# Kernel tuning notes

Measured on AMD Instinct MI355X. Metric: run time of the kernel, lower is better.

## Reference

```python
import jax, jax.numpy as jnp
import numpy as np

B, N, D = 4, 2048, 1024
H = 16
DH = D // H


def setup_inputs() -> dict:
    key = jax.random.key(0)
    ks = jax.random.split(key, 9)
    s_in = 1.0 / np.sqrt(D)
    x = jax.random.normal(ks[0], (B, N, D), dtype=jnp.float32)
    Wq = jax.random.uniform(ks[1], (D, D), jnp.float32, -s_in, s_in)
    bq = jax.random.uniform(ks[2], (D,), jnp.float32, -s_in, s_in)
    Wk = jax.random.uniform(ks[3], (D, D), jnp.float32, -s_in, s_in)
    bk = jax.random.uniform(ks[4], (D,), jnp.float32, -s_in, s_in)
    Wv = jax.random.uniform(ks[5], (D, D), jnp.float32, -s_in, s_in)
    bv = jax.random.uniform(ks[6], (D,), jnp.float32, -s_in, s_in)
    Wo = jax.random.uniform(ks[7], (D, D), jnp.float32, -s_in, s_in)
    bo = jax.random.uniform(ks[8], (D,), jnp.float32, -s_in, s_in)
    return {"x": x, "Wq": Wq, "bq": bq, "Wk": Wk, "bk": bk,
            "Wv": Wv, "bv": bv, "Wo": Wo, "bo": bo}


def reference(x, Wq, bq, Wk, bk, Wv, bv, Wo, bo):
    b, n, d = x.shape
    q = (x @ Wq + bq).reshape(b, n, H, DH)  # (b, n, h, dh)
    k = (x @ Wk + bk).reshape(b, n, H, DH)
    v = (x @ Wv + bv).reshape(b, n, H, DH)
    scale = 1.0 / jnp.sqrt(jnp.asarray(DH, x.dtype))
    scores = jnp.einsum("bqhd,bkhd->bhqk", q, k) * scale  # (b, h, n, n)
    # valid = arange(1..n) per query => causal mask: key index < valid[q] = q+1
    causal = jnp.arange(n)[None, :] <= jnp.arange(n)[:, None]  # (n_q, n_k)
    scores = jnp.where(causal[None, None, :, :], scores, -jnp.inf)
    weights = jax.nn.softmax(scores, axis=-1)
    out = jnp.einsum("bhqk,bkhd->bqhd", weights, v).reshape(b, n, d)
    return out @ Wo + bo
```

## Files before the change

### kernel.cpp

```cpp
#include <hip/hip_runtime.h>
#include <hip/hip_bf16.h>
#include <math.h>

namespace {
constexpr int B_ = 4, N_ = 2048, D_ = 1024, H_ = 16, DH_ = 64;
constexpr int M_ = B_ * N_;
}

typedef __bf16 bf16x8 __attribute__((ext_vector_type(8)));
typedef __bf16 bf16x4 __attribute__((ext_vector_type(4)));
typedef float  f32x4  __attribute__((ext_vector_type(4)));

__device__ inline void async_copy16(const void* g, void* l) {
    __builtin_amdgcn_global_load_lds(
        (const __attribute__((address_space(1))) unsigned int*)g,
        (__attribute__((address_space(3))) unsigned int*)l, 16, 0, 0);
}

__device__ inline float fast_exp2(float x) {
#if __has_builtin(__builtin_amdgcn_exp2f)
    return __builtin_amdgcn_exp2f(x);
#else
    return exp2f(x);
#endif
}

__device__ inline int swz(int row, int c) {
    return c ^ (row & 3) ^ ((row >> 2) & 3);
}

__global__ __launch_bounds__(256) void cast_x(
        const float* __restrict__ x, __bf16* __restrict__ xb)
{
    const size_t i = ((size_t)blockIdx.x * 256 + threadIdx.x) * 8;
    const float4 a = *reinterpret_cast<const float4*>(x + i);
    const float4 b = *reinterpret_cast<const float4*>(x + i + 4);
    bf16x8 o;
    o[0] = (__bf16)a.x; o[1] = (__bf16)a.y; o[2] = (__bf16)a.z; o[3] = (__bf16)a.w;
    o[4] = (__bf16)b.x; o[5] = (__bf16)b.y; o[6] = (__bf16)b.z; o[7] = (__bf16)b.w;
    *reinterpret_cast<bf16x8*>(xb + i) = o;
}

__global__ __launch_bounds__(256) void cast_w(
        const float* __restrict__ Wq, const float* __restrict__ Wk,
        const float* __restrict__ Wv, const float* __restrict__ Wo,
        __bf16* __restrict__ wqkvt, __bf16* __restrict__ wot)
{
    __shared__ float t[64][65];
    const int z = blockIdx.z;
    const float* W = (z == 0) ? Wq : (z == 1) ? Wk : (z == 2) ? Wv : Wo;
    __bf16* dst = (z < 3) ? (wqkvt + (size_t)z * D_ * D_) : wot;
    const int k0 = blockIdx.x * 64, n0 = blockIdx.y * 64;
    const int tid = threadIdx.x;
    #pragma unroll
    for (int p = 0; p < 16; ++p) {
        const int idx = p * 256 + tid;
        const int r = idx >> 6, c = idx & 63;
        t[r][c] = W[(size_t)(k0 + r) * D_ + n0 + c];
    }
    __syncthreads();
    #pragma unroll
    for (int p = 0; p < 16; ++p) {
        const int idx = p * 256 + tid;
        const int r = idx >> 6, c = idx & 63;
        dst[(size_t)(n0 + r) * D_ + k0 + c] = (__bf16)t[c][r];
    }
}

__global__ __launch_bounds__(512, 2) void qkv_mfma(
        const __bf16* __restrict__ A, const __bf16* __restrict__ Bt,
        const float* __restrict__ bq, const float* __restrict__ bk,
        const float* __restrict__ bv,
        __bf16* __restrict__ qo, __bf16* __restrict__ ko, __bf16* __restrict__ vo)
{
    __shared__ __align__(16) __bf16 As[2][256 * 64];
    __shared__ __align__(16) __bf16 Bs[2][256 * 64];
    const int tid = threadIdx.x;
    const int w = tid >> 6, lane = tid & 63;
    const int l15 = lane & 15, quad = lane >> 4;
    const int wr = w >> 2, wc = w & 3;
    const int tm = blockIdx.x * 256;
    const int bn = blockIdx.y * 256;

    const __bf16* Ag = A + (size_t)tm * D_;
    const __bf16* Bg = Bt + (size_t)bn * D_;

    f32x4 acc[8][4] = {};

    auto stage = [&](int t) {
        const int k0 = t * 64;
        __bf16* Ad = As[t & 1];
        __bf16* Bd = Bs[t & 1];
        #pragma unroll
        for (int s = 0; s < 4; ++s) {
            const int idx = s * 512 + tid;
            const int r = idx >> 3, cs = idx & 7;
            const int cl = cs ^ (r & 7);
            async_copy16(Ag + (size_t)r * D_ + k0 + cl * 8, Ad + idx * 8);
        }
        #pragma unroll
        for (int s = 0; s < 4; ++s) {
            const int idx = s * 512 + tid;
            const int r = idx >> 3, cs = idx & 7;
            const int cl = cs ^ (r & 7);
            async_copy16(Bg + (size_t)r * D_ + k0 + cl * 8, Bd + idx * 8);
        }
    };

    stage(0);
    stage(1);
    asm volatile("s_waitcnt vmcnt(8)" ::: "memory");
    __builtin_amdgcn_s_barrier();
    __builtin_amdgcn_sched_barrier(0);

    for (int t = 0; t < 16; ++t) {
        const __bf16* Ab = As[t & 1];
        const __bf16* Bb = Bs[t & 1];
        #pragma unroll
        for (int q = 0; q < 4; ++q) {
            const int ar0 = wr * 128 + (q >> 1) * 64;
            const int bc0 = wc * 64 + (q & 1) * 32;
            bf16x8 af[4][2], bf[2][2];
            #pragma unroll
            for (int fr = 0; fr < 4; ++fr) {
                const int row = ar0 + fr * 16 + l15;
                #pragma unroll
                for (int ks = 0; ks < 2; ++ks)
                    af[fr][ks] = *reinterpret_cast<const bf16x8*>(
                        Ab + row * 64 + ((ks * 4 + quad) ^ (row & 7)) * 8);
            }
            #pragma unroll
            for (int nc = 0; nc < 2; ++nc) {
                const int col = bc0 + nc * 16 + l15;
                #pragma unroll
                for (int ks = 0; ks < 2; ++ks)
                    bf[nc][ks] = *reinterpret_cast<const bf16x8*>(
                        Bb + col * 64 + ((ks * 4 + quad) ^ (col & 7)) * 8);
            }
            __builtin_amdgcn_s_setprio(1);
            #pragma unroll
            for (int fr = 0; fr < 4; ++fr)
                #pragma unroll
                for (int nc = 0; nc < 2; ++nc) {
                    f32x4 c = acc[(q >> 1) * 4 + fr][(q & 1) * 2 + nc];
                    c = __builtin_amdgcn_mfma_f32_16x16x32_bf16(af[fr][0], bf[nc][0], c, 0, 0, 0);
                    c = __builtin_amdgcn_mfma_f32_16x16x32_bf16(af[fr][1], bf[nc][1], c, 0, 0, 0);
                    acc[(q >> 1) * 4 + fr][(q & 1) * 2 + nc] = c;
                }
            __builtin_amdgcn_s_setprio(0);
            __builtin_amdgcn_s_barrier();
        }
        if (t < 14) {
            stage(t + 2);
            asm volatile("s_waitcnt vmcnt(8)" ::: "memory");
        } else if (t == 14) {
            asm volatile("s_waitcnt vmcnt(0)" ::: "memory");
        }
        if (t < 15) {
            __builtin_amdgcn_s_barrier();
            __builtin_amdgcn_sched_barrier(0);
        }
    }

    const int z = blockIdx.y >> 2;
    const float* bias = (z == 0) ? bq : (z == 1) ? bk : bv;
    const int ysec = blockIdx.y & 3;
    const int h = ysec * 4 + wc;
    float bcol[4];
    #pragma unroll
    for (int nc = 0; nc < 4; ++nc) bcol[nc] = bias[h * 64 + nc * 16 + l15];
    const int gr0 = tm + wr * 128;

    if (z < 2) {
        __bf16* dst = (z == 0) ? qo : ko;
        const float sc = (z == 0) ? 0.125f * 1.44269504f : 1.0f;
        #pragma unroll
        for (int mr = 0; mr < 8; ++mr)
            #pragma unroll
            for (int i = 0; i < 4; ++i) {
                const int gr = gr0 + mr * 16 + quad * 4 + i;
                const int b = gr >> 11, tok = gr & (N_ - 1);
                __bf16* row = dst + ((size_t)(b * H_ + h) * N_ + tok) * DH_;
                #pragma unroll
                for (int nc = 0; nc < 4; ++nc)
                    row[nc * 16 + l15] = (__bf16)((acc[mr][nc][i] + bcol[nc]) * sc);
            }
    } else {
        #pragma unroll
        for (int mr = 0; mr < 8; ++mr) {
            const int gr = gr0 + mr * 16 + quad * 4;
            const int b = gr >> 11, tok = gr & (N_ - 1);
            #pragma unroll
            for (int nc = 0; nc < 4; ++nc) {
                const int dh = nc * 16 + l15;
                bf16x4 pv;
                #pragma unroll
                for (int i = 0; i < 4; ++i)
                    pv[i] = (__bf16)(acc[mr][nc][i] + bcol[nc]);
                *reinterpret_cast<bf16x4*>(
                    vo + ((size_t)(b * H_ + h) * DH_ + dh) * N_ + tok) = pv;
            }
        }
    }
}

__global__ __launch_bounds__(256) void out_mfma(
        const __bf16* __restrict__ A, const __bf16* __restrict__ Bt,
        const float* __restrict__ bias, float* __restrict__ out)
{
    __shared__ __align__(16) __bf16 As[128 * 32];
    __shared__ __align__(16) __bf16 Bs[128 * 32];
    const int tid = threadIdx.x;
    const int w = tid >> 6, lane = tid & 63;
    const int l15 = lane & 15, quad = lane >> 4;
    const int tm = blockIdx.x * 128;
    const int tn = blockIdx.y * 128;

    f32x4 acc[4][4] = {};

    for (int k0 = 0; k0 < D_; k0 += 32) {
        __syncthreads();
        #pragma unroll
        for (int it = 0; it < 2; ++it) {
            const int c = it * 256 + tid;
            const int r = c >> 2, pc = c & 3;
            const int lc = swz(r, pc);
            async_copy16(A + (size_t)(tm + r) * D_ + k0 + lc * 8, As + c * 8);
            async_copy16(Bt + (size_t)(tn + r) * D_ + k0 + lc * 8, Bs + c * 8);
        }
        __syncthreads();

        bf16x8 af[4], bfr[4];
        #pragma unroll
        for (int t = 0; t < 4; ++t) {
            const int row = (w >> 1) * 64 + t * 16 + l15;
            af[t] = *reinterpret_cast<const bf16x8*>(
                As + (row * 4 + swz(row, quad)) * 8);
            const int col = (w & 1) * 64 + t * 16 + l15;
            bfr[t] = *reinterpret_cast<const bf16x8*>(
                Bs + (col * 4 + swz(col, quad)) * 8);
        }
        #pragma unroll
        for (int mt = 0; mt < 4; ++mt)
            #pragma unroll
            for (int nt = 0; nt < 4; ++nt)
                acc[mt][nt] = __builtin_amdgcn_mfma_f32_16x16x32_bf16(
                    af[mt], bfr[nt], acc[mt][nt], 0, 0, 0);
    }

    const int col0 = tn + (w & 1) * 64;
    float bcol[4];
    #pragma unroll
    for (int nt = 0; nt < 4; ++nt) bcol[nt] = bias[col0 + nt * 16 + l15];
    const int gr0 = tm + (w >> 1) * 64;
    #pragma unroll
    for (int mt = 0; mt < 4; ++mt)
        #pragma unroll
        for (int i = 0; i < 4; ++i) {
            const int gr = gr0 + mt * 16 + quad * 4 + i;
            float* row = out + (size_t)gr * D_;
            #pragma unroll
            for (int nt = 0; nt < 4; ++nt)
                row[col0 + nt * 16 + l15] = acc[mt][nt][i] + bcol[nt];
        }
}

__global__ __launch_bounds__(256, 4) void attn(
        const __bf16* __restrict__ Q, const __bf16* __restrict__ K,
        const __bf16* __restrict__ Vt, __bf16* __restrict__ ctx)
{
    const int blk = blockIdx.x;
    const int bh = blk & 63;
    const int qb = ((blk >> 6) + bh) & 15;
    const int tid = threadIdx.x;
    const int w = tid >> 6, lane = tid & 63;
    const int l15 = lane & 15, quad = lane >> 4;
    const int qt0 = qb * 128;

    __shared__ __align__(16) __bf16 Ks[64 * 64];
    __shared__ __align__(16) __bf16 Vs[64 * 64];
    __shared__ __align__(16) __bf16 Ps[4][2][16 * 72];

    bf16x8 bqf[2][2];
    #pragma unroll
    for (int qc = 0; qc < 2; ++qc) {
        const size_t base = ((size_t)bh * N_ + qt0 + w * 32 + qc * 16 + l15) * DH_;
        bqf[qc][0] = *reinterpret_cast<const bf16x8*>(Q + base + quad * 8);
        bqf[qc][1] = *reinterpret_cast<const bf16x8*>(Q + base + 32 + quad * 8);
    }

    f32x4 acc[2][4] = {};
    float l_lane[2] = {0.f, 0.f};

    const __bf16* Kg = K + (size_t)bh * N_ * DH_;
    const __bf16* Vg = Vt + (size_t)bh * DH_ * N_;
    const int nkb = 2 * qb + 2;
    const int sr = lane >> 3;
    const int sc = lane & 7;

    for (int kb = 0; kb < nkb; ++kb) {
        __syncthreads();
        #pragma unroll
        for (int j = 0; j < 2; ++j) {
            const int r = j * 32 + w * 8 + sr;
            const int cl = sc ^ (r & 7);
            async_copy16(Kg + (size_t)(kb * 64 + r) * DH_ + cl * 8,
                         &Ks[(j * 256 + tid) * 8]);
            async_copy16(Vg + (size_t)r * N_ + kb * 64 + cl * 8,
                         &Vs[(j * 256 + tid) * 8]);
        }
        __syncthreads();

        f32x4 st[2][4];
        __builtin_amdgcn_s_setprio(1);
        #pragma unroll
        for (int ct = 0; ct < 4; ++ct) {
            const int row = ct * 16 + l15;
            const bf16x8 ka0 = *reinterpret_cast<const bf16x8*>(
                &Ks[(row * 8 + (quad ^ (row & 7))) * 8]);
            const bf16x8 ka1 = *reinterpret_cast<const bf16x8*>(
                &Ks[(row * 8 + ((quad + 4) ^ (row & 7))) * 8]);
            #pragma unroll
            for (int qc = 0; qc < 2; ++qc) {
                f32x4 t = {};
                t = __builtin_amdgcn_mfma_f32_16x16x32_bf16(ka0, bqf[qc][0], t, 0, 0, 0);
                t = __builtin_amdgcn_mfma_f32_16x16x32_bf16(ka1, bqf[qc][1], t, 0, 0, 0);
                st[qc][ct] = t;
            }
        }
        __builtin_amdgcn_s_setprio(0);
        if (kb >= 2 * qb) {
            #pragma unroll
            for (int qc = 0; qc < 2; ++qc) {
                const int q_glob = qt0 + w * 32 + qc * 16 + l15;
                #pragma unroll
                for (int ct = 0; ct < 4; ++ct)
                    #pragma unroll
                    for (int i = 0; i < 4; ++i) {
                        const int k_glob = kb * 64 + ct * 16 + quad * 4 + i;
                        if (k_glob > q_glob) st[qc][ct][i] = -INFINITY;
                    }
            }
        }

        #pragma unroll
        for (int qc = 0; qc < 2; ++qc) {
            float rs = 0.f;
            #pragma unroll
            for (int ct = 0; ct < 4; ++ct) {
                bf16x4 pk;
                #pragma unroll
                for (int i = 0; i < 4; ++i) {
                    const float p = fast_exp2(st[qc][ct][i]);
                    rs += p;
                    pk[i] = (__bf16)p;
                }
                *reinterpret_cast<bf16x4*>(
                    &Ps[w][qc][l15 * 72 + ct * 16 + quad * 4]) = pk;
            }
            l_lane[qc] += rs;
        }

        bf16x8 pa0[2], pa1[2];
        #pragma unroll
        for (int qc = 0; qc < 2; ++qc) {
            pa0[qc] = *reinterpret_cast<const bf16x8*>(
                &Ps[w][qc][l15 * 72 + quad * 8]);
            pa1[qc] = *reinterpret_cast<const bf16x8*>(
                &Ps[w][qc][l15 * 72 + 32 + quad * 8]);
        }
        __builtin_amdgcn_s_setprio(1);
        #pragma unroll
        for (int ct = 0; ct < 4; ++ct) {
            const int row = ct * 16 + l15;
            const bf16x8 vb0 = *reinterpret_cast<const bf16x8*>(
                &Vs[(row * 8 + (quad ^ (row & 7))) * 8]);
            const bf16x8 vb1 = *reinterpret_cast<const bf16x8*>(
                &Vs[(row * 8 + ((quad + 4) ^ (row & 7))) * 8]);
            #pragma unroll
            for (int qc = 0; qc < 2; ++qc) {
                f32x4 t = acc[qc][ct];
                t = __builtin_amdgcn_mfma_f32_16x16x32_bf16(pa0[qc], vb0, t, 0, 0, 0);
                t = __builtin_amdgcn_mfma_f32_16x16x32_bf16(pa1[qc], vb1, t, 0, 0, 0);
                acc[qc][ct] = t;
            }
        }
        __builtin_amdgcn_s_setprio(0);
    }

    const int b = bh >> 4, h = bh & 15;
    #pragma unroll
    for (int qc = 0; qc < 2; ++qc) {
        float r = l_lane[qc];
        r += __shfl_xor(r, 16);
        r += __shfl_xor(r, 32);
        const float linv = 1.0f / r;
        float lT[4];
        #pragma unroll
        for (int i = 0; i < 4; ++i) lT[i] = __shfl(linv, quad * 4 + i);
        #pragma unroll
        for (int i = 0; i < 4; ++i) {
            const int row = qt0 + w * 32 + qc * 16 + quad * 4 + i;
            __bf16* dst = ctx + ((size_t)b * N_ + row) * D_ + h * DH_;
            #pragma unroll
            for (int ct = 0; ct < 4; ++ct)
                dst[ct * 16 + l15] = (__bf16)(acc[qc][ct][i] * lT[i]);
        }
    }
}

extern "C" void kernel_launch(void* const* d_in, const int* in_sizes, int n_in,
                              void* d_out, int out_size, void* d_ws, size_t ws_size,
                              hipStream_t stream) {
    const float* x  = (const float*)d_in[0];
    const float* Wq = (const float*)d_in[1];
    const float* bq = (const float*)d_in[2];
    const float* Wk = (const float*)d_in[3];
    const float* bk = (const float*)d_in[4];
    const float* Wv = (const float*)d_in[5];
    const float* bv = (const float*)d_in[6];
    const float* Wo = (const float*)d_in[7];
    const float* bo = (const float*)d_in[8];
    float* out = (float*)d_out;

    __bf16* xb    = (__bf16*)d_ws;
    __bf16* wqkvt = xb + (size_t)M_ * D_;
    __bf16* wot   = wqkvt + (size_t)3 * D_ * D_;
    __bf16* q     = wot + (size_t)D_ * D_;
    __bf16* k     = q + (size_t)M_ * D_;
    __bf16* vt    = k + (size_t)M_ * D_;
    __bf16* ctx   = vt + (size_t)M_ * D_;

    cast_x<<<dim3(M_ * D_ / (256 * 8)), 256, 0, stream>>>(x, xb);
    cast_w<<<dim3(16, 16, 4), 256, 0, stream>>>(Wq, Wk, Wv, Wo, wqkvt, wot);
    qkv_mfma<<<dim3(M_ / 256, 3 * D_ / 256), 512, 0, stream>>>(
        xb, wqkvt, bq, bk, bv, q, k, vt);
    attn<<<dim3(1024), 256, 0, stream>>>(q, k, vt, ctx);
    out_mfma<<<dim3(M_ / 128, D_ / 128), 256, 0, stream>>>(ctx, wot, bo, out);
}
```

Before: 267.4 us.

## Interleave half-tile async loads with MFMA phases in QKV GEMM

Replaces whole-tile staging between K-steps in the QKV projection GEMM with finer-grained half-tile async global-to-LDS copies. Each copy is issued inside one of the per-wave compute phases, so loads for upcoming K-slices overlap MFMA work, and the loop is unrolled by two over the double buffer. The aim is to hide global load latency and drop the bulk stage-then-wait stall at each K-step boundary. In exchange the wait-count bookkeeping and buffer reuse become more intricate and are easier to get wrong.

```diff
diff --git a/kernel.cpp b/kernel.cpp
--- a/kernel.cpp
+++ b/kernel.cpp
@@ -87,80 +87,95 @@
 
     f32x4 acc[8][4] = {};
 
-    auto stage = [&](int t) {
+    auto stageAh = [&](int t, int half) {
+        const int slot = t & 1;
         const int k0 = t * 64;
-        __bf16* Ad = As[t & 1];
-        __bf16* Bd = Bs[t & 1];
-        #pragma unroll
-        for (int s = 0; s < 4; ++s) {
-            const int idx = s * 512 + tid;
-            const int r = idx >> 3, cs = idx & 7;
-            const int cl = cs ^ (r & 7);
-            async_copy16(Ag + (size_t)r * D_ + k0 + cl * 8, Ad + idx * 8);
-        }
-        #pragma unroll
-        for (int s = 0; s < 4; ++s) {
-            const int idx = s * 512 + tid;
-            const int r = idx >> 3, cs = idx & 7;
-            const int cl = cs ^ (r & 7);
-            async_copy16(Bg + (size_t)r * D_ + k0 + cl * 8, Bd + idx * 8);
+        #pragma unroll
+        for (int s = 0; s < 2; ++s) {
+            const int li = s * 512 + tid;
+            const int rl = li >> 3, cs = li & 7;
+            const int r = half * 64 + rl + (rl & 64);
+            const int csrc = cs ^ (r & 7);
+            async_copy16(Ag + (size_t)r * D_ + k0 + csrc * 8,
+                         &As[slot][(r * 8 + cs) * 8]);
         }
     };
-
-    stage(0);
-    stage(1);
-    asm volatile("s_waitcnt vmcnt(8)" ::: "memory");
-    __builtin_amdgcn_s_barrier();
-    __builtin_amdgcn_sched_barrier(0);
-
-    for (int t = 0; t < 16; ++t) {
-        const __bf16* Ab = As[t & 1];
-        const __bf16* Bb = Bs[t & 1];
-        #pragma unroll
-        for (int q = 0; q < 4; ++q) {
-            const int ar0 = wr * 128 + (q >> 1) * 64;
-            const int bc0 = wc * 64 + (q & 1) * 32;
-            bf16x8 af[4][2], bf[2][2];
-            #pragma unroll
-            for (int fr = 0; fr < 4; ++fr) {
-                const int row = ar0 + fr * 16 + l15;
-                #pragma unroll
-                for (int ks = 0; ks < 2; ++ks)
-                    af[fr][ks] = *reinterpret_cast<const bf16x8*>(
-                        Ab + row * 64 + ((ks * 4 + quad) ^ (row & 7)) * 8);
-            }
-            #pragma unroll
-            for (int nc = 0; nc < 2; ++nc) {
-                const int col = bc0 + nc * 16 + l15;
-                #pragma unroll
-                for (int ks = 0; ks < 2; ++ks)
-                    bf[nc][ks] = *reinterpret_cast<const bf16x8*>(
-                        Bb + col * 64 + ((ks * 4 + quad) ^ (col & 7)) * 8);
-            }
-            __builtin_amdgcn_s_setprio(1);
-            #pragma unroll
-            for (int fr = 0; fr < 4; ++fr)
-                #pragma unroll
-                for (int nc = 0; nc < 2; ++nc) {
-                    f32x4 c = acc[(q >> 1) * 4 + fr][(q & 1) * 2 + nc];
-                    c = __builtin_amdgcn_mfma_f32_16x16x32_bf16(af[fr][0], bf[nc][0], c, 0, 0, 0);
-                    c = __builtin_amdgcn_mfma_f32_16x16x32_bf16(af[fr][1], bf[nc][1], c, 0, 0, 0);
-                    acc[(q >> 1) * 4 + fr][(q & 1) * 2 + nc] = c;
-                }
-            __builtin_amdgcn_s_setprio(0);
-            __builtin_amdgcn_s_barrier();
-        }
-        if (t < 14) {
-            stage(t + 2);
-            asm volatile("s_waitcnt vmcnt(8)" ::: "memory");
-        } else if (t == 14) {
-            asm volatile("s_waitcnt vmcnt(0)" ::: "memory");
-        }
-        if (t < 15) {
-            __builtin_amdgcn_s_barrier();
-            __builtin_amdgcn_sched_barrier(0);
-        }
-    }
+    auto stageBh = [&](int t, int par) {
+        const int slot = t & 1;
+        const int k0 = t * 64;
+        #pragma unroll
+        for (int s = 0; s < 2; ++s) {
+            const int li = s * 512 + tid;
+            const int cl = li >> 3, cs = li & 7;
+            const int col = (cl & 31) + ((cl >> 5) << 6) + par * 32;
+            const int csrc = cs ^ (col & 7);
+            async_copy16(Bg + (size_t)col * D_ + k0 + csrc * 8,
+                         &Bs[slot][(col * 8 + cs) * 8]);
+        }
+    };
+
+#define QKV_PHASE(Ab, Bb, qq, STAGE_STMT, WAIT_STMT)                          \
+    {                                                                         \
+        const int ar0 = wr * 128 + ((qq) >> 1) * 64;                          \
+        const int bc0 = wc * 64 + ((qq) & 1) * 32;                            \
+        bf16x8 af[4][2], bfv[2][2];                                           \
+        _Pragma("unroll")                                                     \
+        for (int fr = 0; fr < 4; ++fr) {                                      \
+            const int row = ar0 + fr * 16 + l15;                              \
+            _Pragma("unroll")                                                 \
+            for (int ks = 0; ks < 2; ++ks)                                    \
+                af[fr][ks] = *reinterpret_cast<const bf16x8*>(                \
+                    (Ab) + row * 64 + (((ks * 4 + quad) ^ (row & 7)) * 8));   \
+        }                                                                     \
+        _Pragma("unroll")                                                     \
+        for (int nc = 0; nc < 2; ++nc) {                                      \
+            const int col = bc0 + nc * 16 + l15;                              \
+            _Pragma("unroll")                                                 \
+            for (int ks = 0; ks < 2; ++ks)                                    \
+                bfv[nc][ks] = *reinterpret_cast<const bf16x8*>(               \
+                    (Bb) + col * 64 + (((ks * 4 + quad) ^ (col & 7)) * 8));   \
+        }                                                                     \
+        STAGE_STMT;                                                           \
+        WAIT_STMT;                                                            \
+        asm volatile("s_barrier" ::: "memory");                               \
+        __builtin_amdgcn_s_setprio(1);                                        \
+        _Pragma("unroll")                                                     \
+        for (int fr = 0; fr < 4; ++fr)                                        \
+            _Pragma("unroll")                                                 \
+            for (int nc = 0; nc < 2; ++nc) {                                  \
+                f32x4 c = acc[((qq) >> 1) * 4 + fr][((qq) & 1) * 2 + nc];     \
+                c = __builtin_amdgcn_mfma_f32_16x16x32_bf16(af[fr][0], bfv[nc][0], c, 0, 0, 0); \
+                c = __builtin_amdgcn_mfma_f32_16x16x32_bf16(af[fr][1], bfv[nc][1], c, 0, 0, 0); \
+                acc[((qq) >> 1) * 4 + fr][((qq) & 1) * 2 + nc] = c;           \
+            }                                                                 \
+        __builtin_amdgcn_s_setprio(0);                                        \
+        asm volatile("s_barrier" ::: "memory");                               \
+    }
+
+    stageAh(0, 0); stageAh(0, 1); stageBh(0, 0); stageBh(0, 1);
+    stageAh(1, 0); stageBh(1, 0);
+    asm volatile("s_waitcnt vmcnt(4)" ::: "memory");
+    asm volatile("s_barrier" ::: "memory");
+
+    for (int i = 0; i < 8; ++i) {
+        const int T1 = 2 * i + 1;
+        const bool more = (i < 7);
+        const __bf16* A0 = As[0]; const __bf16* B0 = Bs[0];
+        const __bf16* A1 = As[1]; const __bf16* B1 = Bs[1];
+
+        QKV_PHASE(A0, B0, 0, stageAh(T1, 1), ((void)0));
+        QKV_PHASE(A0, B0, 1, stageBh(T1, 1), ((void)0));
+        QKV_PHASE(A0, B0, 2, if (more) stageAh(T1 + 1, 0), ((void)0));
+        QKV_PHASE(A0, B0, 3, if (more) stageBh(T1 + 1, 0),
+                  if (more) { asm volatile("s_waitcnt vmcnt(4)" ::: "memory"); }
+                  else      { asm volatile("s_waitcnt vmcnt(0)" ::: "memory"); });
+        QKV_PHASE(A1, B1, 0, if (more) stageAh(T1 + 1, 1), ((void)0));
+        QKV_PHASE(A1, B1, 1, if (more) stageBh(T1 + 1, 1), ((void)0));
+        QKV_PHASE(A1, B1, 2, if (more) stageAh(T1 + 2, 0), ((void)0));
+        QKV_PHASE(A1, B1, 3, if (more) stageBh(T1 + 2, 0),
+                  if (more) { asm volatile("s_waitcnt vmcnt(4)" ::: "memory"); });
+    }
+#undef QKV_PHASE
 
     const int z = blockIdx.y >> 2;
     const float* bias = (z == 0) ? bq : (z == 1) ? bk : bv;
```

Measured after the change: 264.3 us. About the same (-1.1%).
